# Kernel tuning notes

Measured on AMD Instinct MI355X. Metric: run time of the kernel, lower is better.

The kernel has to match this reference:

```python
import jax, jax.numpy as jnp
import numpy as np

B, C, Ci, V = 1024, 256, 128, 90
EPS = 1e-5


def setup_inputs() -> dict:
    key = jax.random.key(0)
    ks = iter(jax.random.split(key, 40))
    def nrm(shape, s=1.0):
        return jax.random.normal(next(ks), shape, jnp.float32) * s
    def uni(shape):
        return jax.random.uniform(next(ks), shape, jnp.float32, 0.5, 1.5)
    inp = {"x1": nrm((B, C, V)), "x2": nrm((B, C, V))}
    for p in ["g", "th", "ph"]:
        inp[p + "_bn_gamma"] = uni((C,))
        inp[p + "_bn_beta"] = nrm((C,), 0.1)
        inp[p + "_bn_mean"] = nrm((C,), 0.1)
        inp[p + "_bn_var"] = uni((C,))
        inp[p + "_w"] = nrm((Ci, C), 0.05)
        inp[p + "_b"] = nrm((Ci,), 0.05)
    inp["W_w"] = nrm((C, Ci), 0.05)
    inp["W_b"] = nrm((C,), 0.05)
    inp["W_bn_gamma"] = uni((C,))
    inp["W_bn_beta"] = nrm((C,), 0.1)
    inp["W_bn_mean"] = nrm((C,), 0.1)
    inp["W_bn_var"] = uni((C,))
    inp["qt_w"] = nrm((Ci, C), 0.05); inp["qt_b"] = nrm((Ci,), 0.05)
    inp["ks_w"] = nrm((Ci, V), 0.05); inp["ks_b"] = nrm((Ci,), 0.05)
    inp["qs_w"] = nrm((Ci, V), 0.05); inp["qs_b"] = nrm((Ci,), 0.05)
    inp["kt_w"] = nrm((Ci, C), 0.05); inp["kt_b"] = nrm((Ci,), 0.05)
    return inp


def _bn(x, g, b, m, v):
    # eval-mode BatchNorm1d over channel dim of (B, C, V)
    return (x - m[:, None]) * jax.lax.rsqrt(v[:, None] + EPS) * g[:, None] + b[:, None]


def _conv1(x, w, b):
    # 1x1 Conv1d: (B, Cin, V) x (Cout, Cin) -> (B, Cout, V)
    return jnp.einsum('bcv,oc->bov', x, w) + b[:, None]


def reference(x1, x2,
              g_bn_gamma, g_bn_beta, g_bn_mean, g_bn_var, g_w, g_b,
              th_bn_gamma, th_bn_beta, th_bn_mean, th_bn_var, th_w, th_b,
              ph_bn_gamma, ph_bn_beta, ph_bn_mean, ph_bn_var, ph_w, ph_b,
              W_w, W_b, W_bn_gamma, W_bn_beta, W_bn_mean, W_bn_var,
              qt_w, qt_b, ks_w, ks_b, qs_w, qs_b, kt_w, kt_b):
    g_x1 = _conv1(_bn(x1, g_bn_gamma, g_bn_beta, g_bn_mean, g_bn_var), g_w, g_b)
    g_x2 = _conv1(_bn(x2, g_bn_gamma, g_bn_beta, g_bn_mean, g_bn_var), g_w, g_b)
    theta = _conv1(_bn(x1, th_bn_gamma, th_bn_beta, th_bn_mean, th_bn_var), th_w, th_b)  # theta(x1)
    phi = _conv1(_bn(x2, ph_bn_gamma, ph_bn_beta, ph_bn_mean, ph_bn_var), ph_w, ph_b)    # phi(x2)

    e_time = jnp.einsum('biv,bjv->bij', theta, phi)   # (B, Ci, Ci) = theta_x1 @ phi_x2
    e_space = jnp.einsum('bci,bcj->bij', theta, phi)  # (B, V, V)  = theta_x2 @ phi_x1

    attn_time_1 = jax.nn.softmax(e_time, axis=-1)
    attn_time_2 = jax.nn.softmax(jnp.swapaxes(e_time, 1, 2), axis=-1)
    attn_space_2 = jax.nn.softmax(e_space, axis=-1)
    attn_space_1 = jax.nn.softmax(jnp.swapaxes(e_space, 1, 2), axis=-1)

    z1 = jnp.einsum('bij,bjv,bvw->biw', attn_time_2, g_x1, attn_space_2)  # (B, Ci, V)
    z2 = jnp.einsum('bij,bjv,bvw->biw', attn_time_1, g_x2, attn_space_1)

    m1t = x1.mean(axis=2)                      # (B, C)
    q_time = m1t @ qt_w.T + qt_b               # (B, Ci)
    k_space = x2.mean(axis=1) @ ks_w.T + ks_b  # (B, Ci)
    # bmm of (B,1,Ci) x (B,Ci,1) -> (B,1,1); softmax over singleton dim == 1 (kept for faithfulness)
    attn_t2s = jax.nn.softmax(jnp.sum(q_time * k_space, axis=-1, keepdims=True)[:, :, None], axis=-1)
    x2n = x2 + attn_t2s * m1t[:, :, None]      # broadcast (B,1,1)*(B,C,1) over V

    q_space = x1.mean(axis=1) @ qs_w.T + qs_b  # (B, Ci)
    k_time = x2n.mean(axis=2) @ kt_w.T + kt_b  # (B, Ci)
    attn_s2t = jax.nn.softmax(jnp.sum(q_space * k_time, axis=-1, keepdims=True)[:, :, None], axis=-1)
    x1n = x1 + attn_s2t * x2n.mean(axis=1)[:, None, :]

    def Wop(z):
        return _bn(_conv1(z, W_w, W_b), W_bn_gamma, W_bn_beta, W_bn_mean, W_bn_var)

    return (x1n + Wop(z1), x2n + Wop(z2))
```

## Files before the change

kernel.cpp:

```cpp
#include <hip/hip_runtime.h>

namespace {

constexpr int B = 1024;

using u16 = unsigned short;
using u32 = unsigned int;

typedef __attribute__((ext_vector_type(8))) short bf16x8;
typedef __attribute__((ext_vector_type(4))) float f32x4;

#define MFMA16(a, b, c) __builtin_amdgcn_mfma_f32_16x16x32_bf16(a, b, c, 0, 0, 0)

__device__ __forceinline__ u16 f2bf(float f) {
  u32 u = __builtin_bit_cast(u32, f);
  u += 0x7FFFu + ((u >> 16) & 1u);
  return (u16)(u >> 16);
}
__device__ __forceinline__ float bf2f(u16 s) {
  u32 u = ((u32)s) << 16;
  return __builtin_bit_cast(float, u);
}
__device__ __forceinline__ u32 packbf2(float a, float b) {
  return (u32)f2bf(a) | ((u32)f2bf(b) << 16);
}

__global__ __launch_bounds__(256) void k0_fold(
    const float* __restrict__ gg, const float* __restrict__ gbe, const float* __restrict__ gme, const float* __restrict__ gva,
    const float* __restrict__ gw, const float* __restrict__ gbi,
    const float* __restrict__ tg, const float* __restrict__ tbe, const float* __restrict__ tme, const float* __restrict__ tva,
    const float* __restrict__ tw, const float* __restrict__ tbi,
    const float* __restrict__ pg, const float* __restrict__ pbe, const float* __restrict__ pme, const float* __restrict__ pva,
    const float* __restrict__ pw, const float* __restrict__ pbi,
    const float* __restrict__ Ww, const float* __restrict__ Wb,
    const float* __restrict__ Wg2, const float* __restrict__ Wbe, const float* __restrict__ Wme, const float* __restrict__ Wva,
    u16* __restrict__ wgo, float* __restrict__ bgo,
    u16* __restrict__ wthi, u16* __restrict__ wtlo, float* __restrict__ bto,
    u16* __restrict__ wphi, u16* __restrict__ wplo, float* __restrict__ bpo,
    u16* __restrict__ wWo, float* __restrict__ bWo)
{
  __shared__ float red[4];
  const int blk = blockIdx.x, tid = threadIdx.x;
  if (blk < 384) {
    const int p = blk >> 7, o = blk & 127;
    const float *ga, *be, *me, *va, *wm, *bi;
    if (p == 0)      { ga = gg; be = gbe; me = gme; va = gva; wm = gw; bi = gbi; }
    else if (p == 1) { ga = tg; be = tbe; me = tme; va = tva; wm = tw; bi = tbi; }
    else             { ga = pg; be = pbe; me = pme; va = pva; wm = pw; bi = pbi; }
    float s = ga[tid] * rsqrtf(va[tid] + 1e-5f);
    float t = be[tid] - me[tid] * s;
    float wv = wm[o * 256 + tid];
    float val = wv * s;
    if (p == 0) {
      wgo[o * 256 + tid] = f2bf(val);
    } else {
      u16 hi = f2bf(val);
      u16 lo = f2bf(val - bf2f(hi));
      if (p == 1) { wthi[o * 256 + tid] = hi; wtlo[o * 256 + tid] = lo; }
      else        { wphi[o * 256 + tid] = hi; wplo[o * 256 + tid] = lo; }
    }
    float part = t * wv;
#pragma unroll
    for (int off = 32; off; off >>= 1) part += __shfl_down(part, off);
    if ((tid & 63) == 0) red[tid >> 6] = part;
    __syncthreads();
    if (tid == 0) {
      float bsum = bi[o] + red[0] + red[1] + red[2] + red[3];
      if (p == 0) bgo[o] = bsum; else if (p == 1) bto[o] = bsum; else bpo[o] = bsum;
    }
  } else {
    const int c = blk - 384;
    float sW = Wg2[c] * rsqrtf(Wva[c] + 1e-5f);
    if (tid < 128) wWo[c * 128 + tid] = f2bf(Ww[c * 128 + tid] * sW);
    if (tid == 0) bWo[c] = Wb[c] * sW + Wbe[c] - Wme[c] * sW;
  }
}

__global__ __launch_bounds__(512) void k1_conv(
    const float* __restrict__ x1, const float* __restrict__ x2,
    const u16* __restrict__ wG, const float* __restrict__ bG,
    const u16* __restrict__ wTh, const u16* __restrict__ wTl, const float* __restrict__ bT,
    const u16* __restrict__ wPh, const u16* __restrict__ wPl, const float* __restrict__ bP,
    float* __restrict__ thT, float* __restrict__ phT,
    u16* __restrict__ gout,
    float* __restrict__ m1t, float* __restrict__ x2cm, float* __restrict__ x1am)
{
  __shared__ u16 xhi[96 * 264];
  __shared__ u16 xlo[96 * 264];
  __shared__ float red[8];
  const int b = blockIdx.x, tid = threadIdx.x;
  const int l = tid & 63, wv = tid >> 6;
  const int lr = l & 15, lq = l >> 4;
  const int c = tid >> 1, h = tid & 1;

  const float* xb1 = x1 + (size_t)b * 23040;
  const float* xb2 = x2 + (size_t)b * 23040;
  u16* g1d = gout + (size_t)b * 46080;
  u16* g2d = gout + (size_t)(1024 + b) * 46080;
  float* thTb = thT + (size_t)b * 11520;
  float* phTb = phT + (size_t)b * 11520;

  const f32x4 zero = {0.f, 0.f, 0.f, 0.f};

  auto stage = [&](const float* __restrict__ xb) -> float {
    float s = 0.f;
    const int v2lo = h ? 23 : 0, v2hi = h ? 45 : 23;
    for (int v2 = v2lo; v2 < v2hi; ++v2) {
      float2 f = *(const float2*)(xb + c * 90 + 2 * v2);
      s += f.x + f.y;
      u16 h0 = f2bf(f.x);
      xhi[(2 * v2) * 264 + c] = h0;
      xlo[(2 * v2) * 264 + c] = f2bf(f.x - bf2f(h0));
      u16 h1 = f2bf(f.y);
      xhi[(2 * v2 + 1) * 264 + c] = h1;
      xlo[(2 * v2 + 1) * 264 + c] = f2bf(f.y - bf2f(h1));
    }
    for (int i = tid; i < 1536; i += 512) {
      int v = 90 + (i >> 8), cc = i & 255;
      xhi[v * 264 + cc] = 0; xlo[v * 264 + cc] = 0;
    }
    return s;
  };

  auto convSplit = [&](const u16* __restrict__ Wh, const u16* __restrict__ Wl,
                       const float* __restrict__ bias, float* __restrict__ dstF) {
    const int mt = wv;
    f32x4 acc[6];
#pragma unroll
    for (int i = 0; i < 6; ++i) acc[i] = zero;
#pragma unroll
    for (int kk = 0; kk < 8; ++kk) {
      bf16x8 ah = *(const bf16x8*)(Wh + (16 * mt + lr) * 256 + kk * 32 + 8 * lq);
      bf16x8 al = *(const bf16x8*)(Wl + (16 * mt + lr) * 256 + kk * 32 + 8 * lq);
#pragma unroll
      for (int nt = 0; nt < 6; ++nt) {
        bf16x8 bh = *(const bf16x8*)&xhi[(16 * nt + lr) * 264 + kk * 32 + 8 * lq];
        bf16x8 bl = *(const bf16x8*)&xlo[(16 * nt + lr) * 264 + kk * 32 + 8 * lq];
        acc[nt] = MFMA16(ah, bh, acc[nt]);
        acc[nt] = MFMA16(ah, bl, acc[nt]);
        acc[nt] = MFMA16(al, bh, acc[nt]);
      }
    }
    const int c0 = 16 * mt + 4 * lq;
    const float4 b4 = *(const float4*)(bias + c0);
#pragma unroll
    for (int nt = 0; nt < 6; ++nt) {
      const int v = 16 * nt + lr;
      if (v < 90) {
        float4 o;
        o.x = acc[nt][0] + b4.x; o.y = acc[nt][1] + b4.y;
        o.z = acc[nt][2] + b4.z; o.w = acc[nt][3] + b4.w;
        *(float4*)(dstF + v * 128 + c0) = o;
      }
    }
  };

  auto convG = [&](const u16* __restrict__ Wm, const float* __restrict__ bias, u16* __restrict__ dst) {
    const int mt = wv;
    f32x4 acc[6];
#pragma unroll
    for (int i = 0; i < 6; ++i) acc[i] = zero;
#pragma unroll
    for (int kk = 0; kk < 8; ++kk) {
      bf16x8 a = *(const bf16x8*)(Wm + (16 * mt + lr) * 256 + kk * 32 + 8 * lq);
#pragma unroll
      for (int nt = 0; nt < 6; ++nt) {
        bf16x8 bb = *(const bf16x8*)&xhi[(16 * nt + lr) * 264 + kk * 32 + 8 * lq];
        acc[nt] = MFMA16(a, bb, acc[nt]);
      }
    }
    const int c0 = 16 * mt + 4 * lq;
    const float4 b4 = *(const float4*)(bias + c0);
#pragma unroll
    for (int nt = 0; nt < 6; ++nt) {
      const int v = 16 * nt + lr;
      uint2 pk;
      if (v < 90) {
        pk.x = packbf2(acc[nt][0] + b4.x, acc[nt][1] + b4.y);
        pk.y = packbf2(acc[nt][2] + b4.z, acc[nt][3] + b4.w);
      } else { pk.x = 0u; pk.y = 0u; }
      *(uint2*)(dst + v * 128 + c0) = pk;
    }
  };

  {
    float s = stage(xb1);
    float s2 = s + __shfl_down(s, 1);
    if (h == 0) m1t[b * 256 + c] = s2 * (1.f / 90.f);
    float t = s;
#pragma unroll
    for (int o = 32; o; o >>= 1) t += __shfl_down(t, o);
    if (l == 0) red[wv] = t;
  }
  __syncthreads();
  if (tid == 0) {
    float a = 0.f;
#pragma unroll
    for (int i = 0; i < 8; ++i) a += red[i];
    x1am[b] = a * (1.f / 23040.f);
  }
  convSplit(wTh, wTl, bT, thTb);
  convG(wG, bG, g1d);
  __syncthreads();
  stage(xb2);
  __syncthreads();
  if (tid < 96) {
    float s = 0.f;
    for (int cc = 0; cc < 256; ++cc)
      s += bf2f(xhi[tid * 264 + cc]) + bf2f(xlo[tid * 264 + cc]);
    x2cm[b * 96 + tid] = s * (1.f / 256.f);
  }
  convSplit(wPh, wPl, bP, phTb);
  convG(wG, bG, g2d);
}

__global__ __launch_bounds__(256) void k2_attn(
    const float* __restrict__ thTg_, const float* __restrict__ phTg_,
    u16* __restrict__ At1g, u16* __restrict__ At2g,
    u16* __restrict__ As1g, u16* __restrict__ As2g)
{
  __shared__ __align__(16) char smem[108544];
  u16* s0 = (u16*)smem;
  float* st = (float*)(smem + 106496);
  float* eL = (float*)smem;

  const int b = blockIdx.x, tid = threadIdx.x;
  const int l = tid & 63, wv = tid >> 6, lr = l & 15, lq = l >> 4;
  const float* thg = thTg_ + (size_t)b * 11520;
  const float* phg = phTg_ + (size_t)b * 11520;
  const f32x4 zero = {0.f, 0.f, 0.f, 0.f};

  u16* th_hi = s0;
  u16* th_lo = s0 + 13312;
  u16* ph_hi = s0 + 26624;
  u16* ph_lo = s0 + 39936;
  for (int d = tid; d < 2880; d += 256) {
    int v = d >> 5, cq = d & 31;
    float4 t4 = *(const float4*)(thg + v * 128 + 4 * cq);
    float4 p4 = *(const float4*)(phg + v * 128 + 4 * cq);
    float ta[4] = {t4.x, t4.y, t4.z, t4.w};
    float pa[4] = {p4.x, p4.y, p4.z, p4.w};
#pragma unroll
    for (int k = 0; k < 4; ++k) {
      int ci = 4 * cq + k;
      u16 thh = f2bf(ta[k]);
      th_hi[ci * 104 + v] = thh;
      th_lo[ci * 104 + v] = f2bf(ta[k] - bf2f(thh));
      u16 phh = f2bf(pa[k]);
      ph_hi[ci * 104 + v] = phh;
      ph_lo[ci * 104 + v] = f2bf(pa[k] - bf2f(phh));
    }
  }
  for (int d = tid; d < 768; d += 256) {
    int ci = d / 6, v = 90 + d % 6;
    th_hi[ci * 104 + v] = 0; th_lo[ci * 104 + v] = 0;
    ph_hi[ci * 104 + v] = 0; ph_lo[ci * 104 + v] = 0;
  }
  __syncthreads();
  f32x4 accT[2][8];
#pragma unroll
  for (int mi = 0; mi < 2; ++mi)
#pragma unroll
    for (int nt = 0; nt < 8; ++nt) accT[mi][nt] = zero;
#pragma unroll
  for (int mi = 0; mi < 2; ++mi) {
    const int mt = 2 * wv + mi;
#pragma unroll
    for (int kk = 0; kk < 3; ++kk) {
      bf16x8 ah = *(const bf16x8*)&th_hi[(16 * mt + lr) * 104 + kk * 32 + 8 * lq];
      bf16x8 al = *(const bf16x8*)&th_lo[(16 * mt + lr) * 104 + kk * 32 + 8 * lq];
#pragma unroll
      for (int nt = 0; nt < 8; ++nt) {
        bf16x8 bh = *(const bf16x8*)&ph_hi[(16 * nt + lr) * 104 + kk * 32 + 8 * lq];
        bf16x8 bl = *(const bf16x8*)&ph_lo[(16 * nt + lr) * 104 + kk * 32 + 8 * lq];
        accT[mi][nt] = MFMA16(ah, bh, accT[mi][nt]);
        accT[mi][nt] = MFMA16(ah, bl, accT[mi][nt]);
        accT[mi][nt] = MFMA16(al, bh, accT[mi][nt]);
      }
    }
  }
  __syncthreads();
#pragma unroll
  for (int mi = 0; mi < 2; ++mi) {
    const int mt = 2 * wv + mi;
#pragma unroll
    for (int nt = 0; nt < 8; ++nt)
#pragma unroll
      for (int r = 0; r < 4; ++r)
        eL[(16 * nt + lr) * 133 + 16 * mt + 4 * lq + r] = accT[mi][nt][r];
  }
  __syncthreads();
  if (tid < 128) {
    int j = tid; float m = -1e30f;
    for (int i = 0; i < 128; ++i) m = fmaxf(m, eL[j * 133 + i]);
    float s = 0.f;
    for (int i = 0; i < 128; ++i) s += __expf(eL[j * 133 + i] - m);
    st[j] = m; st[128 + j] = 1.f / s;
  } else {
    int i = tid - 128; float m = -1e30f;
    for (int j = 0; j < 128; ++j) m = fmaxf(m, eL[j * 133 + i]);
    float s = 0.f;
    for (int j = 0; j < 128; ++j) s += __expf(eL[j * 133 + i] - m);
    st[256 + i] = m; st[384 + i] = 1.f / s;
  }
  __syncthreads();
  {
    u32* A1 = (u32*)(At1g + (size_t)b * 16384);
    u32* A2 = (u32*)(At2g + (size_t)b * 16384);
    for (int d = tid; d < 8192; d += 256) {
      int i = d >> 6, jp = d & 63;
      float m1 = st[256 + i], s1 = st[384 + i];
      float a0 = __expf(eL[(2 * jp) * 133 + i] - m1) * s1;
      float a1 = __expf(eL[(2 * jp + 1) * 133 + i] - m1) * s1;
      A1[d] = packbf2(a0, a1);
      float m2 = st[i], s2 = st[128 + i];
      float b0 = __expf(eL[i * 133 + 2 * jp] - m2) * s2;
      float b1 = __expf(eL[i * 133 + 2 * jp + 1] - m2) * s2;
      A2[d] = packbf2(b0, b1);
    }
  }
  __syncthreads();

  u16* tTh = s0;
  u16* tTl = s0 + 13056;
  u16* pTh = s0 + 26112;
  u16* pTl = s0 + 39168;
  for (int d = tid; d < 2880; d += 256) {
    int v = d >> 5, cq = d & 31;
    float4 t4 = *(const float4*)(thg + v * 128 + 4 * cq);
    float4 p4 = *(const float4*)(phg + v * 128 + 4 * cq);
    float ta[4] = {t4.x, t4.y, t4.z, t4.w};
    float pa[4] = {p4.x, p4.y, p4.z, p4.w};
    u16 th_h[4], th_l[4], ph_h[4], ph_l[4];
#pragma unroll
    for (int k = 0; k < 4; ++k) {
      th_h[k] = f2bf(ta[k]); th_l[k] = f2bf(ta[k] - bf2f(th_h[k]));
      ph_h[k] = f2bf(pa[k]); ph_l[k] = f2bf(pa[k] - bf2f(ph_h[k]));
    }
    uint2 w0, w1;
    w0.x = (u32)th_h[0] | ((u32)th_h[1] << 16); w0.y = (u32)th_h[2] | ((u32)th_h[3] << 16);
    *(uint2*)&tTh[v * 136 + 4 * cq] = w0;
    w1.x = (u32)th_l[0] | ((u32)th_l[1] << 16); w1.y = (u32)th_l[2] | ((u32)th_l[3] << 16);
    *(uint2*)&tTl[v * 136 + 4 * cq] = w1;
    w0.x = (u32)ph_h[0] | ((u32)ph_h[1] << 16); w0.y = (u32)ph_h[2] | ((u32)ph_h[3] << 16);
    *(uint2*)&pTh[v * 136 + 4 * cq] = w0;
    w1.x = (u32)ph_l[0] | ((u32)ph_l[1] << 16); w1.y = (u32)ph_l[2] | ((u32)ph_l[3] << 16);
    *(uint2*)&pTl[v * 136 + 4 * cq] = w1;
  }
  for (int d = tid; d < 192; d += 256) {
    int v = 90 + (d >> 5), cq = d & 31;
    uint2 z; z.x = 0u; z.y = 0u;
    *(uint2*)&tTh[v * 136 + 4 * cq] = z;
    *(uint2*)&tTl[v * 136 + 4 * cq] = z;
    *(uint2*)&pTh[v * 136 + 4 * cq] = z;
    *(uint2*)&pTl[v * 136 + 4 * cq] = z;
  }
  __syncthreads();
  f32x4 accS[9];
#pragma unroll
  for (int it = 0; it < 9; ++it) accS[it] = zero;
#pragma unroll
  for (int it = 0; it < 9; ++it) {
    const int t5 = wv + 4 * it;
    const int mt = t5 / 6, nt = t5 - 6 * (t5 / 6);
#pragma unroll
    for (int kk = 0; kk < 4; ++kk) {
      bf16x8 ah = *(const bf16x8*)&tTh[(16 * mt + lr) * 136 + kk * 32 + 8 * lq];
      bf16x8 al = *(const bf16x8*)&tTl[(16 * mt + lr) * 136 + kk * 32 + 8 * lq];
      bf16x8 bh = *(const bf16x8*)&pTh[(16 * nt + lr) * 136 + kk * 32 + 8 * lq];
      bf16x8 bl = *(const bf16x8*)&pTl[(16 * nt + lr) * 136 + kk * 32 + 8 * lq];
      accS[it] = MFMA16(ah, bh, accS[it]);
      accS[it] = MFMA16(ah, bl, accS[it]);
      accS[it] = MFMA16(al, bh, accS[it]);
    }
  }
  __syncthreads();
  {
    float* esL = (float*)smem;
#pragma unroll
    for (int it = 0; it < 9; ++it) {
      const int t5 = wv + 4 * it;
      const int mt = t5 / 6, nt = t5 - 6 * (t5 / 6);
#pragma unroll
      for (int r = 0; r < 4; ++r)
        esL[(16 * nt + lr) * 101 + 16 * mt + 4 * lq + r] = accS[it][r];
    }
  }
  __syncthreads();
  {
    float* esL = (float*)smem;
    if (tid < 96) {
      int v = tid; float m = -1e30f;
      for (int w2 = 0; w2 < 90; ++w2) m = fmaxf(m, esL[v * 101 + w2]);
      float s = 0.f;
      for (int w2 = 0; w2 < 90; ++w2) s += __expf(esL[v * 101 + w2] - m);
      st[v] = m; st[128 + v] = 1.f / s;
    } else if (tid >= 128 && tid < 224) {
      int v = tid - 128; float m = -1e30f;
      for (int w2 = 0; w2 < 90; ++w2) m = fmaxf(m, esL[w2 * 101 + v]);
      float s = 0.f;
      for (int w2 = 0; w2 < 90; ++w2) s += __expf(esL[w2 * 101 + v] - m);
      st[256 + v] = m; st[384 + v] = 1.f / s;
    }
  }
  __syncthreads();
  {
    float* esL = (float*)smem;
    u32* S1 = (u32*)(As1g + (size_t)b * 9216);
    u32* S2 = (u32*)(As2g + (size_t)b * 9216);
    for (int d = tid; d < 4608; d += 256) {
      int w2 = d / 48, vp = d - (d / 48) * 48;
      int v0 = 2 * vp, v1 = 2 * vp + 1;
      float a0 = __expf(esL[v0 * 101 + w2] - st[v0]) * st[128 + v0];
      float a1 = __expf(esL[v1 * 101 + w2] - st[v1]) * st[128 + v1];
      S1[d] = packbf2(a0, a1);
      float b0 = __expf(esL[w2 * 101 + v0] - st[256 + v0]) * st[384 + v0];
      float b1 = __expf(esL[w2 * 101 + v1] - st[256 + v1]) * st[384 + v1];
      S2[d] = packbf2(b0, b1);
    }
  }
}

__global__ __launch_bounds__(256) void k3_out(
    const float* __restrict__ x1, const float* __restrict__ x2,
    const u16* __restrict__ At1g, const u16* __restrict__ At2g,
    const u16* __restrict__ As1g, const u16* __restrict__ As2g,
    const u16* __restrict__ wW, const float* __restrict__ bW,
    const float* __restrict__ m1t, const float* __restrict__ x2cm, const float* __restrict__ x1am,
    float* __restrict__ out)
{
  __shared__ u16 gT[96 * 136];
  __shared__ u16 Tb[128 * 104];
  __shared__ u16 ZT[96 * 136];
  const int b = blockIdx.x, tid = threadIdx.x;
  const int l = tid & 63, wv = tid >> 6, lr = l & 15, lq = l >> 4;
  const f32x4 zero = {0.f, 0.f, 0.f, 0.f};

  float* out1 = out + (size_t)b * 23040;
  float* out2 = out + (size_t)23040 * 1024 + (size_t)b * 23040;
  const u16* g1s = (const u16*)out1;
  const u16* g2s = (const u16*)out2;

  auto phase = [&](const u16* __restrict__ gsrc, const u16* __restrict__ At,
                   const u16* __restrict__ AsT, const float* __restrict__ xres,
                   float* __restrict__ dst, bool modeA) {
    for (int i = tid; i < 1536; i += 256) {
      int v = i >> 4, hh = i & 15;
      *(uint4*)&gT[v * 136 + 8 * hh] = ((const uint4*)gsrc)[i];
    }
    __syncthreads();
#pragma unroll
    for (int ni = 0; ni < 2; ++ni) {
      const int nt = 2 * wv + ni;
      f32x4 acc[6];
#pragma unroll
      for (int i = 0; i < 6; ++i) acc[i] = zero;
#pragma unroll
      for (int kk = 0; kk < 4; ++kk) {
        bf16x8 bb = *(const bf16x8*)(At + (16 * nt + lr) * 128 + kk * 32 + 8 * lq);
#pragma unroll
        for (int mt = 0; mt < 6; ++mt) {
          bf16x8 a = *(const bf16x8*)&gT[(16 * mt + lr) * 136 + kk * 32 + 8 * lq];
          acc[mt] = MFMA16(a, bb, acc[mt]);
        }
      }
#pragma unroll
      for (int mt = 0; mt < 6; ++mt) {
        uint2 pk;
        pk.x = packbf2(acc[mt][0], acc[mt][1]);
        pk.y = packbf2(acc[mt][2], acc[mt][3]);
        *(uint2*)&Tb[(16 * nt + lr) * 104 + 16 * mt + 4 * lq] = pk;
      }
    }
    __syncthreads();
    {
      f32x4 acc[2][6];
#pragma unroll
      for (int i = 0; i < 2; ++i)
#pragma unroll
        for (int j = 0; j < 6; ++j) acc[i][j] = zero;
#pragma unroll
      for (int kk = 0; kk < 3; ++kk) {
        bf16x8 a0 = *(const bf16x8*)&Tb[(16 * (2 * wv) + lr) * 104 + kk * 32 + 8 * lq];
        bf16x8 a1 = *(const bf16x8*)&Tb[(16 * (2 * wv + 1) + lr) * 104 + kk * 32 + 8 * lq];
#pragma unroll
        for (int nt = 0; nt < 6; ++nt) {
          bf16x8 bb = *(const bf16x8*)(AsT + (16 * nt + lr) * 96 + kk * 32 + 8 * lq);
          acc[0][nt] = MFMA16(a0, bb, acc[0][nt]);
          acc[1][nt] = MFMA16(a1, bb, acc[1][nt]);
        }
      }
#pragma unroll
      for (int mi = 0; mi < 2; ++mi) {
        const int mt = 2 * wv + mi;
#pragma unroll
        for (int nt = 0; nt < 6; ++nt) {
          uint2 pk;
          pk.x = packbf2(acc[mi][nt][0], acc[mi][nt][1]);
          pk.y = packbf2(acc[mi][nt][2], acc[mi][nt][3]);
          *(uint2*)&ZT[(16 * nt + lr) * 136 + 16 * mt + 4 * lq] = pk;
        }
      }
    }
    __syncthreads();
    const float am = modeA ? 0.f : x1am[b];
#pragma unroll
    for (int mi = 0; mi < 4; ++mi) {
      const int mt = 4 * wv + mi;
      f32x4 acc[6];
#pragma unroll
      for (int i = 0; i < 6; ++i) acc[i] = zero;
#pragma unroll
      for (int kk = 0; kk < 4; ++kk) {
        bf16x8 a = *(const bf16x8*)(wW + (16 * mt + lr) * 128 + kk * 32 + 8 * lq);
#pragma unroll
        for (int nt = 0; nt < 6; ++nt) {
          bf16x8 bb = *(const bf16x8*)&ZT[(16 * nt + lr) * 136 + kk * 32 + 8 * lq];
          acc[nt] = MFMA16(a, bb, acc[nt]);
        }
      }
      const int c0 = 16 * mt + 4 * lq;
      const float4 bw4 = *(const float4*)(bW + c0);
      float bwA[4] = {bw4.x, bw4.y, bw4.z, bw4.w};
      float mA[4] = {0.f, 0.f, 0.f, 0.f};
      if (modeA) {
        const float4 m4 = *(const float4*)(m1t + b * 256 + c0);
        mA[0] = m4.x; mA[1] = m4.y; mA[2] = m4.z; mA[3] = m4.w;
      }
#pragma unroll
      for (int nt = 0; nt < 6; ++nt) {
        const int v = 16 * nt + lr;
        if (v < 90) {
          const float addv = modeA ? 0.f : (am + x2cm[b * 96 + v]);
#pragma unroll
          for (int r = 0; r < 4; ++r) {
            const int c = c0 + r;
            const float extra = modeA ? mA[r] : addv;
            dst[c * 90 + v] = xres[c * 90 + v] + acc[nt][r] + bwA[r] + extra;
          }
        }
      }
    }
    __syncthreads();
  };

  phase(g2s, At1g + (size_t)b * 16384, As1g + (size_t)b * 9216,
        x2 + (size_t)b * 23040, out2, true);
  phase(g1s, At2g + (size_t)b * 16384, As2g + (size_t)b * 9216,
        x1 + (size_t)b * 23040, out1, false);
}

}

extern "C" void kernel_launch(void* const* d_in, const int* in_sizes, int n_in,
                              void* d_out, int out_size, void* d_ws, size_t ws_size,
                              hipStream_t stream)
{
  (void)in_sizes; (void)n_in; (void)out_size; (void)ws_size;
  const float* x1  = (const float*)d_in[0];
  const float* x2  = (const float*)d_in[1];
  const float* gg  = (const float*)d_in[2];
  const float* gbe = (const float*)d_in[3];
  const float* gme = (const float*)d_in[4];
  const float* gva = (const float*)d_in[5];
  const float* gw  = (const float*)d_in[6];
  const float* gbi = (const float*)d_in[7];
  const float* tg  = (const float*)d_in[8];
  const float* tbe = (const float*)d_in[9];
  const float* tme = (const float*)d_in[10];
  const float* tva = (const float*)d_in[11];
  const float* tw  = (const float*)d_in[12];
  const float* tbi = (const float*)d_in[13];
  const float* pg  = (const float*)d_in[14];
  const float* pbe = (const float*)d_in[15];
  const float* pme = (const float*)d_in[16];
  const float* pva = (const float*)d_in[17];
  const float* pw  = (const float*)d_in[18];
  const float* pbi = (const float*)d_in[19];
  const float* Ww  = (const float*)d_in[20];
  const float* Wb  = (const float*)d_in[21];
  const float* Wg  = (const float*)d_in[22];
  const float* Wbe = (const float*)d_in[23];
  const float* Wme = (const float*)d_in[24];
  const float* Wva = (const float*)d_in[25];

  float* out = (float*)d_out;
  unsigned char* W8 = (unsigned char*)d_ws;

  size_t off = 0;
  auto al = [&](size_t n) { size_t r = off; off += (n + 255) & ~(size_t)255; return r; };
  const size_t oWG  = al(65536);
  const size_t oWTh = al(65536), oWTl = al(65536);
  const size_t oWPh = al(65536), oWPl = al(65536);
  const size_t oWW  = al(65536);
  const size_t oBG = al(512), oBT = al(512), oBP = al(512), oBW = al(1024);
  const size_t oTH = al((size_t)B * 46080), oPH = al((size_t)B * 46080);
  const size_t oA1 = al((size_t)B * 32768), oA2 = al((size_t)B * 32768);
  const size_t oS1 = al((size_t)B * 18432), oS2 = al((size_t)B * 18432);
  const size_t oM1 = al((size_t)B * 1024), oXC = al((size_t)B * 384), oXA = al((size_t)B * 4);

  k0_fold<<<dim3(640), dim3(256), 0, stream>>>(
      gg, gbe, gme, gva, gw, gbi,
      tg, tbe, tme, tva, tw, tbi,
      pg, pbe, pme, pva, pw, pbi,
      Ww, Wb, Wg, Wbe, Wme, Wva,
      (u16*)(W8 + oWG), (float*)(W8 + oBG),
      (u16*)(W8 + oWTh), (u16*)(W8 + oWTl), (float*)(W8 + oBT),
      (u16*)(W8 + oWPh), (u16*)(W8 + oWPl), (float*)(W8 + oBP),
      (u16*)(W8 + oWW), (float*)(W8 + oBW));

  k1_conv<<<dim3(B), dim3(512), 0, stream>>>(
      x1, x2,
      (const u16*)(W8 + oWG), (const float*)(W8 + oBG),
      (const u16*)(W8 + oWTh), (const u16*)(W8 + oWTl), (const float*)(W8 + oBT),
      (const u16*)(W8 + oWPh), (const u16*)(W8 + oWPl), (const float*)(W8 + oBP),
      (float*)(W8 + oTH), (float*)(W8 + oPH),
      (u16*)out,
      (float*)(W8 + oM1), (float*)(W8 + oXC), (float*)(W8 + oXA));

  k2_attn<<<dim3(B), dim3(256), 0, stream>>>(
      (const float*)(W8 + oTH), (const float*)(W8 + oPH),
      (u16*)(W8 + oA1), (u16*)(W8 + oA2),
      (u16*)(W8 + oS1), (u16*)(W8 + oS2));

  k3_out<<<dim3(B), dim3(256), 0, stream>>>(
      x1, x2,
      (const u16*)(W8 + oA1), (const u16*)(W8 + oA2),
      (const u16*)(W8 + oS1), (const u16*)(W8 + oS2),
      (const u16*)(W8 + oWW), (const float*)(W8 + oBW),
      (const float*)(W8 + oM1), (const float*)(W8 + oXC), (const float*)(W8 + oXA),
      out);
}
```

Measured before the change: 463.9 us.

## Restage conv in channel halves, emit pre-split bf16 theta/phi, widen attention kernel

k1_conv now stages x in two 128-channel halves through a smaller shared buffer, allowing more blocks per CU, and fuses the theta/phi and g convolutions into one MFMA loop. It writes theta/phi already split into packed bf16 hi/lo words in two layouts: channel-major in workspace and v-major in spare space of the output buffer. This removes the fp32 reload and resplitting in k2_attn. k2_attn moves to 512 threads, and the spatial attention maps are stored inside the output buffer instead of separate workspace, relying on k3 reading them before it overwrites that region.

```diff
diff --git a/kernel.cpp b/kernel.cpp
--- a/kernel.cpp
+++ b/kernel.cpp
@@ -76,148 +76,144 @@
   }
 }
 
-__global__ __launch_bounds__(512) void k1_conv(
+__global__ __launch_bounds__(512, 4) void k1_conv(
     const float* __restrict__ x1, const float* __restrict__ x2,
     const u16* __restrict__ wG, const float* __restrict__ bG,
     const u16* __restrict__ wTh, const u16* __restrict__ wTl, const float* __restrict__ bT,
     const u16* __restrict__ wPh, const u16* __restrict__ wPl, const float* __restrict__ bP,
-    float* __restrict__ thT, float* __restrict__ phT,
-    u16* __restrict__ gout,
+    u32* __restrict__ thRm, u32* __restrict__ phRm,
+    u16* __restrict__ outU,
     float* __restrict__ m1t, float* __restrict__ x2cm, float* __restrict__ x1am)
 {
-  __shared__ u16 xhi[96 * 264];
-  __shared__ u16 xlo[96 * 264];
-  __shared__ float red[8];
+  __shared__ u32 qb[64 * 92];
+  __shared__ u16 xh[96 * 136];
+  __shared__ u16 xl[96 * 136];
+  __shared__ float red[4];
   const int b = blockIdx.x, tid = threadIdx.x;
-  const int l = tid & 63, wv = tid >> 6;
-  const int lr = l & 15, lq = l >> 4;
-  const int c = tid >> 1, h = tid & 1;
-
-  const float* xb1 = x1 + (size_t)b * 23040;
-  const float* xb2 = x2 + (size_t)b * 23040;
-  u16* g1d = gout + (size_t)b * 46080;
-  u16* g2d = gout + (size_t)(1024 + b) * 46080;
-  float* thTb = thT + (size_t)b * 11520;
-  float* phTb = phT + (size_t)b * 11520;
-
+  const int l = tid & 63, wv = tid >> 6, lr = l & 15, lq = l >> 4;
   const f32x4 zero = {0.f, 0.f, 0.f, 0.f};
 
-  auto stage = [&](const float* __restrict__ xb) -> float {
-    float s = 0.f;
-    const int v2lo = h ? 23 : 0, v2hi = h ? 45 : 23;
-    for (int v2 = v2lo; v2 < v2hi; ++v2) {
-      float2 f = *(const float2*)(xb + c * 90 + 2 * v2);
-      s += f.x + f.y;
-      u16 h0 = f2bf(f.x);
-      xhi[(2 * v2) * 264 + c] = h0;
-      xlo[(2 * v2) * 264 + c] = f2bf(f.x - bf2f(h0));
-      u16 h1 = f2bf(f.y);
-      xhi[(2 * v2 + 1) * 264 + c] = h1;
-      xlo[(2 * v2 + 1) * 264 + c] = f2bf(f.y - bf2f(h1));
-    }
-    for (int i = tid; i < 1536; i += 512) {
-      int v = 90 + (i >> 8), cc = i & 255;
-      xhi[v * 264 + cc] = 0; xlo[v * 264 + cc] = 0;
-    }
-    return s;
-  };
-
-  auto convSplit = [&](const u16* __restrict__ Wh, const u16* __restrict__ Wl,
-                       const float* __restrict__ bias, float* __restrict__ dstF) {
-    const int mt = wv;
-    f32x4 acc[6];
-#pragma unroll
-    for (int i = 0; i < 6; ++i) acc[i] = zero;
-#pragma unroll
-    for (int kk = 0; kk < 8; ++kk) {
-      bf16x8 ah = *(const bf16x8*)(Wh + (16 * mt + lr) * 256 + kk * 32 + 8 * lq);
-      bf16x8 al = *(const bf16x8*)(Wl + (16 * mt + lr) * 256 + kk * 32 + 8 * lq);
-#pragma unroll
-      for (int nt = 0; nt < 6; ++nt) {
-        bf16x8 bh = *(const bf16x8*)&xhi[(16 * nt + lr) * 264 + kk * 32 + 8 * lq];
-        bf16x8 bl = *(const bf16x8*)&xlo[(16 * nt + lr) * 264 + kk * 32 + 8 * lq];
-        acc[nt] = MFMA16(ah, bh, acc[nt]);
-        acc[nt] = MFMA16(ah, bl, acc[nt]);
-        acc[nt] = MFMA16(al, bh, acc[nt]);
-      }
-    }
-    const int c0 = 16 * mt + 4 * lq;
-    const float4 b4 = *(const float4*)(bias + c0);
+  auto doPhase = [&](const float* __restrict__ xb,
+                     const u16* __restrict__ Wh, const u16* __restrict__ Wl, const float* __restrict__ biasT,
+                     u32* __restrict__ rmDst, u32* __restrict__ pkDst, u16* __restrict__ gDst, bool isX1) {
+    f32x4 aT[6], aG[6];
+#pragma unroll
+    for (int i = 0; i < 6; ++i) { aT[i] = zero; aG[i] = zero; }
+    float cs = 0.f;
+    for (int h = 0; h < 2; ++h) {
+      for (int q = 0; q < 2; ++q) {
+        __syncthreads();
+        const float* src = xb + (2 * h + q) * 5760;
+        for (int t = tid; t < 2880; t += 512) {
+          float2 f = *(const float2*)(src + 2 * t);
+          int cl = (2 * t) / 90, v = 2 * t - 90 * cl;
+          u16 h0 = f2bf(f.x); u16 l0 = f2bf(f.x - bf2f(h0));
+          u16 h1 = f2bf(f.y); u16 l1 = f2bf(f.y - bf2f(h1));
+          uint2 w; w.x = (u32)h0 | ((u32)l0 << 16); w.y = (u32)h1 | ((u32)l1 << 16);
+          *(uint2*)&qb[cl * 92 + v] = w;
+        }
+        __syncthreads();
+        for (int t = tid; t < 1440; t += 512) {
+          int v = t % 90, c4 = t / 90;
+          u32 p0 = qb[(4 * c4 + 0) * 92 + v], p1 = qb[(4 * c4 + 1) * 92 + v];
+          u32 p2 = qb[(4 * c4 + 2) * 92 + v], p3 = qb[(4 * c4 + 3) * 92 + v];
+          uint2 hi, lo;
+          hi.x = (p0 & 0xFFFFu) | (p1 << 16);
+          hi.y = (p2 & 0xFFFFu) | (p3 << 16);
+          lo.x = (p0 >> 16) | (p1 & 0xFFFF0000u);
+          lo.y = (p2 >> 16) | (p3 & 0xFFFF0000u);
+          int base = v * 136 + 64 * q + 4 * c4;
+          *(uint2*)&xh[base] = hi;
+          *(uint2*)&xl[base] = lo;
+        }
+        if (q == 1) {
+          for (int t = tid; t < 384; t += 512) {
+            int v = 90 + (t >> 6), c2 = (t & 63) * 2;
+            *(u32*)&xh[v * 136 + c2] = 0u;
+            *(u32*)&xl[v * 136 + c2] = 0u;
+          }
+        }
+      }
+      __syncthreads();
+      if (isX1) {
+        if (tid < 128) {
+          float s = 0.f;
+          for (int v = 0; v < 90; ++v) s += bf2f(xh[v * 136 + tid]) + bf2f(xl[v * 136 + tid]);
+          m1t[b * 256 + 128 * h + tid] = s * (1.f / 90.f);
+#pragma unroll
+          for (int o = 32; o; o >>= 1) s += __shfl_down(s, o);
+          if ((tid & 63) == 0) red[(tid >> 6) + 2 * h] = s;
+        }
+      } else {
+        if (tid < 90) {
+          float s = 0.f;
+          for (int cl = 0; cl < 128; ++cl) s += bf2f(xh[tid * 136 + cl]) + bf2f(xl[tid * 136 + cl]);
+          cs += s;
+        }
+      }
+      for (int kk = 0; kk < 4; ++kk) {
+        const int wo = (16 * wv + lr) * 256 + 128 * h + kk * 32 + 8 * lq;
+        bf16x8 ah = *(const bf16x8*)(Wh + wo);
+        bf16x8 al = *(const bf16x8*)(Wl + wo);
+        bf16x8 ag = *(const bf16x8*)(wG + wo);
+#pragma unroll
+        for (int nt = 0; nt < 6; ++nt) {
+          const int bo = (16 * nt + lr) * 136 + kk * 32 + 8 * lq;
+          bf16x8 bh = *(const bf16x8*)&xh[bo];
+          bf16x8 bl = *(const bf16x8*)&xl[bo];
+          aT[nt] = MFMA16(ah, bh, aT[nt]);
+          aT[nt] = MFMA16(ah, bl, aT[nt]);
+          aT[nt] = MFMA16(al, bh, aT[nt]);
+          aG[nt] = MFMA16(ag, bh, aG[nt]);
+        }
+      }
+    }
+    __syncthreads();
+    const int c0 = 16 * wv + 4 * lq;
+    const float4 bt4 = *(const float4*)(biasT + c0);
+    const float4 bg4 = *(const float4*)(bG + c0);
 #pragma unroll
     for (int nt = 0; nt < 6; ++nt) {
       const int v = 16 * nt + lr;
+      u32 pk0, pk1, pk2, pk3; uint2 gpk;
       if (v < 90) {
-        float4 o;
-        o.x = acc[nt][0] + b4.x; o.y = acc[nt][1] + b4.y;
-        o.z = acc[nt][2] + b4.z; o.w = acc[nt][3] + b4.w;
-        *(float4*)(dstF + v * 128 + c0) = o;
-      }
+        float t0 = aT[nt][0] + bt4.x, t1 = aT[nt][1] + bt4.y;
+        float t2 = aT[nt][2] + bt4.z, t3 = aT[nt][3] + bt4.w;
+        u16 h0 = f2bf(t0), h1 = f2bf(t1), h2 = f2bf(t2), h3 = f2bf(t3);
+        pk0 = (u32)h0 | ((u32)f2bf(t0 - bf2f(h0)) << 16);
+        pk1 = (u32)h1 | ((u32)f2bf(t1 - bf2f(h1)) << 16);
+        pk2 = (u32)h2 | ((u32)f2bf(t2 - bf2f(h2)) << 16);
+        pk3 = (u32)h3 | ((u32)f2bf(t3 - bf2f(h3)) << 16);
+        gpk.x = packbf2(aG[nt][0] + bg4.x, aG[nt][1] + bg4.y);
+        gpk.y = packbf2(aG[nt][2] + bg4.z, aG[nt][3] + bg4.w);
+      } else { pk0 = pk1 = pk2 = pk3 = 0u; gpk.x = 0u; gpk.y = 0u; }
+      uint4 q4; q4.x = pk0; q4.y = pk1; q4.z = pk2; q4.w = pk3;
+      *(uint4*)(pkDst + v * 128 + c0) = q4;
+      rmDst[(c0 + 0) * 96 + v] = pk0;
+      rmDst[(c0 + 1) * 96 + v] = pk1;
+      rmDst[(c0 + 2) * 96 + v] = pk2;
+      rmDst[(c0 + 3) * 96 + v] = pk3;
+      *(uint2*)(gDst + v * 128 + c0) = gpk;
+    }
+    if (isX1) {
+      if (tid == 0) x1am[b] = (red[0] + red[1] + red[2] + red[3]) * (1.f / 23040.f);
+    } else {
+      if (tid < 90) x2cm[b * 96 + tid] = cs * (1.f / 256.f);
     }
   };
 
-  auto convG = [&](const u16* __restrict__ Wm, const float* __restrict__ bias, u16* __restrict__ dst) {
-    const int mt = wv;
-    f32x4 acc[6];
-#pragma unroll
-    for (int i = 0; i < 6; ++i) acc[i] = zero;
-#pragma unroll
-    for (int kk = 0; kk < 8; ++kk) {
-      bf16x8 a = *(const bf16x8*)(Wm + (16 * mt + lr) * 256 + kk * 32 + 8 * lq);
-#pragma unroll
-      for (int nt = 0; nt < 6; ++nt) {
-        bf16x8 bb = *(const bf16x8*)&xhi[(16 * nt + lr) * 264 + kk * 32 + 8 * lq];
-        acc[nt] = MFMA16(a, bb, acc[nt]);
-      }
-    }
-    const int c0 = 16 * mt + 4 * lq;
-    const float4 b4 = *(const float4*)(bias + c0);
-#pragma unroll
-    for (int nt = 0; nt < 6; ++nt) {
-      const int v = 16 * nt + lr;
-      uint2 pk;
-      if (v < 90) {
-        pk.x = packbf2(acc[nt][0] + b4.x, acc[nt][1] + b4.y);
-        pk.y = packbf2(acc[nt][2] + b4.z, acc[nt][3] + b4.w);
-      } else { pk.x = 0u; pk.y = 0u; }
-      *(uint2*)(dst + v * 128 + c0) = pk;
-    }
-  };
-
-  {
-    float s = stage(xb1);
-    float s2 = s + __shfl_down(s, 1);
-    if (h == 0) m1t[b * 256 + c] = s2 * (1.f / 90.f);
-    float t = s;
-#pragma unroll
-    for (int o = 32; o; o >>= 1) t += __shfl_down(t, o);
-    if (l == 0) red[wv] = t;
-  }
-  __syncthreads();
-  if (tid == 0) {
-    float a = 0.f;
-#pragma unroll
-    for (int i = 0; i < 8; ++i) a += red[i];
-    x1am[b] = a * (1.f / 23040.f);
-  }
-  convSplit(wTh, wTl, bT, thTb);
-  convG(wG, bG, g1d);
-  __syncthreads();
-  stage(xb2);
-  __syncthreads();
-  if (tid < 96) {
-    float s = 0.f;
-    for (int cc = 0; cc < 256; ++cc)
-      s += bf2f(xhi[tid * 264 + cc]) + bf2f(xlo[tid * 264 + cc]);
-    x2cm[b * 96 + tid] = s * (1.f / 256.f);
-  }
-  convSplit(wPh, wPl, bP, phTb);
-  convG(wG, bG, g2d);
-}
-
-__global__ __launch_bounds__(256) void k2_attn(
-    const float* __restrict__ thTg_, const float* __restrict__ phTg_,
-    u16* __restrict__ At1g, u16* __restrict__ At2g,
-    u16* __restrict__ As1g, u16* __restrict__ As2g)
+  u16* o1 = outU + (size_t)b * 46080;
+  u16* o2 = outU + (size_t)(1024 + b) * 46080;
+  doPhase(x1 + (size_t)b * 23040, wTh, wTl, bT,
+          thRm + (size_t)b * 12288, (u32*)(o1 + 12288), o1, true);
+  doPhase(x2 + (size_t)b * 23040, wPh, wPl, bP,
+          phRm + (size_t)b * 12288, (u32*)(o2 + 12288), o2, false);
+}
+
+__global__ __launch_bounds__(512) void k2_attn(
+    const u32* __restrict__ thRm, const u32* __restrict__ phRm,
+    u16* __restrict__ outU,
+    u16* __restrict__ At1g, u16* __restrict__ At2g)
 {
   __shared__ __align__(16) char smem[108544];
   u16* s0 = (u16*)smem;
@@ -226,69 +222,57 @@
 
   const int b = blockIdx.x, tid = threadIdx.x;
   const int l = tid & 63, wv = tid >> 6, lr = l & 15, lq = l >> 4;
-  const float* thg = thTg_ + (size_t)b * 11520;
-  const float* phg = phTg_ + (size_t)b * 11520;
   const f32x4 zero = {0.f, 0.f, 0.f, 0.f};
+
+  const u32* thRmB = thRm + (size_t)b * 12288;
+  const u32* phRmB = phRm + (size_t)b * 12288;
+  const u32* thPk = (const u32*)(outU + (size_t)b * 46080 + 12288);
+  const u32* phPk = (const u32*)(outU + (size_t)(1024 + b) * 46080 + 12288);
+  u32* S1 = (u32*)(outU + (size_t)(1024 + b) * 46080 + 36864);
+  u32* S2 = (u32*)(outU + (size_t)b * 46080 + 36864);
 
   u16* th_hi = s0;
   u16* th_lo = s0 + 13312;
   u16* ph_hi = s0 + 26624;
   u16* ph_lo = s0 + 39936;
-  for (int d = tid; d < 2880; d += 256) {
-    int v = d >> 5, cq = d & 31;
-    float4 t4 = *(const float4*)(thg + v * 128 + 4 * cq);
-    float4 p4 = *(const float4*)(phg + v * 128 + 4 * cq);
-    float ta[4] = {t4.x, t4.y, t4.z, t4.w};
-    float pa[4] = {p4.x, p4.y, p4.z, p4.w};
-#pragma unroll
-    for (int k = 0; k < 4; ++k) {
-      int ci = 4 * cq + k;
-      u16 thh = f2bf(ta[k]);
-      th_hi[ci * 104 + v] = thh;
-      th_lo[ci * 104 + v] = f2bf(ta[k] - bf2f(thh));
-      u16 phh = f2bf(pa[k]);
-      ph_hi[ci * 104 + v] = phh;
-      ph_lo[ci * 104 + v] = f2bf(pa[k] - bf2f(phh));
-    }
-  }
-  for (int d = tid; d < 768; d += 256) {
-    int ci = d / 6, v = 90 + d % 6;
-    th_hi[ci * 104 + v] = 0; th_lo[ci * 104 + v] = 0;
-    ph_hi[ci * 104 + v] = 0; ph_lo[ci * 104 + v] = 0;
-  }
-  __syncthreads();
-  f32x4 accT[2][8];
-#pragma unroll
-  for (int mi = 0; mi < 2; ++mi)
-#pragma unroll
-    for (int nt = 0; nt < 8; ++nt) accT[mi][nt] = zero;
-#pragma unroll
-  for (int mi = 0; mi < 2; ++mi) {
-    const int mt = 2 * wv + mi;
-#pragma unroll
-    for (int kk = 0; kk < 3; ++kk) {
-      bf16x8 ah = *(const bf16x8*)&th_hi[(16 * mt + lr) * 104 + kk * 32 + 8 * lq];
-      bf16x8 al = *(const bf16x8*)&th_lo[(16 * mt + lr) * 104 + kk * 32 + 8 * lq];
-#pragma unroll
-      for (int nt = 0; nt < 8; ++nt) {
-        bf16x8 bh = *(const bf16x8*)&ph_hi[(16 * nt + lr) * 104 + kk * 32 + 8 * lq];
-        bf16x8 bl = *(const bf16x8*)&ph_lo[(16 * nt + lr) * 104 + kk * 32 + 8 * lq];
-        accT[mi][nt] = MFMA16(ah, bh, accT[mi][nt]);
-        accT[mi][nt] = MFMA16(ah, bl, accT[mi][nt]);
-        accT[mi][nt] = MFMA16(al, bh, accT[mi][nt]);
-      }
-    }
-  }
-  __syncthreads();
-#pragma unroll
-  for (int mi = 0; mi < 2; ++mi) {
-    const int mt = 2 * wv + mi;
-#pragma unroll
-    for (int nt = 0; nt < 8; ++nt)
-#pragma unroll
-      for (int r = 0; r < 4; ++r)
-        eL[(16 * nt + lr) * 133 + 16 * mt + 4 * lq + r] = accT[mi][nt][r];
-  }
+  for (int d = tid; d < 6144; d += 512) {
+    int ten = (d >= 3072);
+    int i = d - 3072 * ten;
+    int ci = i / 24, q4 = i - 24 * ci;
+    uint4 P = *(const uint4*)((ten ? phRmB : thRmB) + ci * 96 + 4 * q4);
+    uint2 hi, lo;
+    hi.x = (P.x & 0xFFFFu) | (P.y << 16);
+    hi.y = (P.z & 0xFFFFu) | (P.w << 16);
+    lo.x = (P.x >> 16) | (P.y & 0xFFFF0000u);
+    lo.y = (P.z >> 16) | (P.w & 0xFFFF0000u);
+    *(uint2*)((ten ? ph_hi : th_hi) + ci * 104 + 4 * q4) = hi;
+    *(uint2*)((ten ? ph_lo : th_lo) + ci * 104 + 4 * q4) = lo;
+  }
+  __syncthreads();
+  f32x4 acc[8];
+#pragma unroll
+  for (int nt = 0; nt < 8; ++nt) acc[nt] = zero;
+#pragma unroll
+  for (int kk = 0; kk < 3; ++kk) {
+    const int ao = (16 * wv + lr) * 104 + kk * 32 + 8 * lq;
+    bf16x8 ah = *(const bf16x8*)&th_hi[ao];
+    bf16x8 al = *(const bf16x8*)&th_lo[ao];
+#pragma unroll
+    for (int nt = 0; nt < 8; ++nt) {
+      const int bo = (16 * nt + lr) * 104 + kk * 32 + 8 * lq;
+      bf16x8 bh = *(const bf16x8*)&ph_hi[bo];
+      bf16x8 bl = *(const bf16x8*)&ph_lo[bo];
+      acc[nt] = MFMA16(ah, bh, acc[nt]);
+      acc[nt] = MFMA16(ah, bl, acc[nt]);
+      acc[nt] = MFMA16(al, bh, acc[nt]);
+    }
+  }
+  __syncthreads();
+#pragma unroll
+  for (int nt = 0; nt < 8; ++nt)
+#pragma unroll
+    for (int r = 0; r < 4; ++r)
+      eL[(16 * nt + lr) * 133 + 16 * wv + 4 * lq + r] = acc[nt][r];
   __syncthreads();
   if (tid < 128) {
     int j = tid; float m = -1e30f;
@@ -296,7 +280,7 @@
     float s = 0.f;
     for (int i = 0; i < 128; ++i) s += __expf(eL[j * 133 + i] - m);
     st[j] = m; st[128 + j] = 1.f / s;
-  } else {
+  } else if (tid < 256) {
     int i = tid - 128; float m = -1e30f;
     for (int j = 0; j < 128; ++j) m = fmaxf(m, eL[j * 133 + i]);
     float s = 0.f;
@@ -307,15 +291,15 @@
   {
     u32* A1 = (u32*)(At1g + (size_t)b * 16384);
     u32* A2 = (u32*)(At2g + (size_t)b * 16384);
-    for (int d = tid; d < 8192; d += 256) {
+    for (int d = tid; d < 8192; d += 512) {
       int i = d >> 6, jp = d & 63;
-      float m1 = st[256 + i], s1 = st[384 + i];
-      float a0 = __expf(eL[(2 * jp) * 133 + i] - m1) * s1;
-      float a1 = __expf(eL[(2 * jp + 1) * 133 + i] - m1) * s1;
+      float m1 = st[256 + i], s1v = st[384 + i];
+      float a0 = __expf(eL[(2 * jp) * 133 + i] - m1) * s1v;
+      float a1 = __expf(eL[(2 * jp + 1) * 133 + i] - m1) * s1v;
       A1[d] = packbf2(a0, a1);
-      float m2 = st[i], s2 = st[128 + i];
-      float b0 = __expf(eL[i * 133 + 2 * jp] - m2) * s2;
-      float b1 = __expf(eL[i * 133 + 2 * jp + 1] - m2) * s2;
+      float m2 = st[i], s2v = st[128 + i];
+      float b0 = __expf(eL[i * 133 + 2 * jp] - m2) * s2v;
+      float b1 = __expf(eL[i * 133 + 2 * jp + 1] - m2) * s2v;
       A2[d] = packbf2(b0, b1);
     }
   }
@@ -325,65 +309,54 @@
   u16* tTl = s0 + 13056;
   u16* pTh = s0 + 26112;
   u16* pTl = s0 + 39168;
-  for (int d = tid; d < 2880; d += 256) {
-    int v = d >> 5, cq = d & 31;
-    float4 t4 = *(const float4*)(thg + v * 128 + 4 * cq);
-    float4 p4 = *(const float4*)(phg + v * 128 + 4 * cq);
-    float ta[4] = {t4.x, t4.y, t4.z, t4.w};
-    float pa[4] = {p4.x, p4.y, p4.z, p4.w};
-    u16 th_h[4], th_l[4], ph_h[4], ph_l[4];
-#pragma unroll
-    for (int k = 0; k < 4; ++k) {
-      th_h[k] = f2bf(ta[k]); th_l[k] = f2bf(ta[k] - bf2f(th_h[k]));
-      ph_h[k] = f2bf(pa[k]); ph_l[k] = f2bf(pa[k] - bf2f(ph_h[k]));
-    }
-    uint2 w0, w1;
-    w0.x = (u32)th_h[0] | ((u32)th_h[1] << 16); w0.y = (u32)th_h[2] | ((u32)th_h[3] << 16);
-    *(uint2*)&tTh[v * 136 + 4 * cq] = w0;
-    w1.x = (u32)th_l[0] | ((u32)th_l[1] << 16); w1.y = (u32)th_l[2] | ((u32)th_l[3] << 16);
-    *(uint2*)&tTl[v * 136 + 4 * cq] = w1;
-    w0.x = (u32)ph_h[0] | ((u32)ph_h[1] << 16); w0.y = (u32)ph_h[2] | ((u32)ph_h[3] << 16);
-    *(uint2*)&pTh[v * 136 + 4 * cq] = w0;
-    w1.x = (u32)ph_l[0] | ((u32)ph_l[1] << 16); w1.y = (u32)ph_l[2] | ((u32)ph_l[3] << 16);
-    *(uint2*)&pTl[v * 136 + 4 * cq] = w1;
-  }
-  for (int d = tid; d < 192; d += 256) {
-    int v = 90 + (d >> 5), cq = d & 31;
-    uint2 z; z.x = 0u; z.y = 0u;
-    *(uint2*)&tTh[v * 136 + 4 * cq] = z;
-    *(uint2*)&tTl[v * 136 + 4 * cq] = z;
-    *(uint2*)&pTh[v * 136 + 4 * cq] = z;
-    *(uint2*)&pTl[v * 136 + 4 * cq] = z;
-  }
-  __syncthreads();
-  f32x4 accS[9];
-#pragma unroll
-  for (int it = 0; it < 9; ++it) accS[it] = zero;
-#pragma unroll
-  for (int it = 0; it < 9; ++it) {
-    const int t5 = wv + 4 * it;
-    const int mt = t5 / 6, nt = t5 - 6 * (t5 / 6);
-#pragma unroll
-    for (int kk = 0; kk < 4; ++kk) {
-      bf16x8 ah = *(const bf16x8*)&tTh[(16 * mt + lr) * 136 + kk * 32 + 8 * lq];
-      bf16x8 al = *(const bf16x8*)&tTl[(16 * mt + lr) * 136 + kk * 32 + 8 * lq];
-      bf16x8 bh = *(const bf16x8*)&pTh[(16 * nt + lr) * 136 + kk * 32 + 8 * lq];
-      bf16x8 bl = *(const bf16x8*)&pTl[(16 * nt + lr) * 136 + kk * 32 + 8 * lq];
-      accS[it] = MFMA16(ah, bh, accS[it]);
-      accS[it] = MFMA16(ah, bl, accS[it]);
-      accS[it] = MFMA16(al, bh, accS[it]);
+  for (int d = tid; d < 6144; d += 512) {
+    int ten = (d >= 3072);
+    int i = d - 3072 * ten;
+    int v = i >> 5, q4 = i & 31;
+    uint4 P = *(const uint4*)((ten ? phPk : thPk) + v * 128 + 4 * q4);
+    uint2 hi, lo;
+    hi.x = (P.x & 0xFFFFu) | (P.y << 16);
+    hi.y = (P.z & 0xFFFFu) | (P.w << 16);
+    lo.x = (P.x >> 16) | (P.y & 0xFFFF0000u);
+    lo.y = (P.z >> 16) | (P.w & 0xFFFF0000u);
+    *(uint2*)((ten ? pTh : tTh) + v * 136 + 4 * q4) = hi;
+    *(uint2*)((ten ? pTl : tTl) + v * 136 + 4 * q4) = lo;
+  }
+  __syncthreads();
+  f32x4 accS[5];
+#pragma unroll
+  for (int it = 0; it < 5; ++it) accS[it] = zero;
+#pragma unroll
+  for (int it = 0; it < 5; ++it) {
+    const int t5 = wv + 8 * it;
+    if (t5 < 36) {
+      const int mt = t5 / 6, nt = t5 - 6 * (t5 / 6);
+#pragma unroll
+      for (int kk = 0; kk < 4; ++kk) {
+        const int ao = (16 * mt + lr) * 136 + kk * 32 + 8 * lq;
+        const int bo = (16 * nt + lr) * 136 + kk * 32 + 8 * lq;
+        bf16x8 ah = *(const bf16x8*)&tTh[ao];
+        bf16x8 al = *(const bf16x8*)&tTl[ao];
+        bf16x8 bh = *(const bf16x8*)&pTh[bo];
+        bf16x8 bl = *(const bf16x8*)&pTl[bo];
+        accS[it] = MFMA16(ah, bh, accS[it]);
+        accS[it] = MFMA16(ah, bl, accS[it]);
+        accS[it] = MFMA16(al, bh, accS[it]);
+      }
     }
   }
   __syncthreads();
   {
     float* esL = (float*)smem;
 #pragma unroll
-    for (int it = 0; it < 9; ++it) {
-      const int t5 = wv + 4 * it;
-      const int mt = t5 / 6, nt = t5 - 6 * (t5 / 6);
-#pragma unroll
-      for (int r = 0; r < 4; ++r)
-        esL[(16 * nt + lr) * 101 + 16 * mt + 4 * lq + r] = accS[it][r];
+    for (int it = 0; it < 5; ++it) {
+      const int t5 = wv + 8 * it;
+      if (t5 < 36) {
+        const int mt = t5 / 6, nt = t5 - 6 * (t5 / 6);
+#pragma unroll
+        for (int r = 0; r < 4; ++r)
+          esL[(16 * nt + lr) * 101 + 16 * mt + 4 * lq + r] = accS[it][r];
+      }
     }
   }
   __syncthreads();
@@ -406,11 +379,9 @@
   __syncthreads();
   {
     float* esL = (float*)smem;
-    u32* S1 = (u32*)(As1g + (size_t)b * 9216);
-    u32* S2 = (u32*)(As2g + (size_t)b * 9216);
-    for (int d = tid; d < 4608; d += 256) {
-      int w2 = d / 48, vp = d - (d / 48) * 48;
-      int v0 = 2 * vp, v1 = 2 * vp + 1;
+    for (int d = tid; d < 4608; d += 512) {
+      int w2 = d / 48, vp = d - 48 * (d / 48);
+      int v0 = 2 * vp, v1 = v0 + 1;
       float a0 = __expf(esL[v0 * 101 + w2] - st[v0]) * st[128 + v0];
       float a1 = __expf(esL[v1 * 101 + w2] - st[v1]) * st[128 + v1];
       S1[d] = packbf2(a0, a1);
@@ -424,7 +395,6 @@
 __global__ __launch_bounds__(256) void k3_out(
     const float* __restrict__ x1, const float* __restrict__ x2,
     const u16* __restrict__ At1g, const u16* __restrict__ At2g,
-    const u16* __restrict__ As1g, const u16* __restrict__ As2g,
     const u16* __restrict__ wW, const float* __restrict__ bW,
     const float* __restrict__ m1t, const float* __restrict__ x2cm, const float* __restrict__ x1am,
     float* __restrict__ out)
@@ -440,6 +410,8 @@
   float* out2 = out + (size_t)23040 * 1024 + (size_t)b * 23040;
   const u16* g1s = (const u16*)out1;
   const u16* g2s = (const u16*)out2;
+  const u16* As1 = (const u16*)out2 + 36864;
+  const u16* As2 = (const u16*)out1 + 36864;
 
   auto phase = [&](const u16* __restrict__ gsrc, const u16* __restrict__ At,
                    const u16* __restrict__ AsT, const float* __restrict__ xres,
@@ -544,10 +516,8 @@
     __syncthreads();
   };
 
-  phase(g2s, At1g + (size_t)b * 16384, As1g + (size_t)b * 9216,
-        x2 + (size_t)b * 23040, out2, true);
-  phase(g1s, At2g + (size_t)b * 16384, As2g + (size_t)b * 9216,
-        x1 + (size_t)b * 23040, out1, false);
+  phase(g2s, At1g + (size_t)b * 16384, As1, x2 + (size_t)b * 23040, out2, true);
+  phase(g1s, At2g + (size_t)b * 16384, As2, x1 + (size_t)b * 23040, out1, false);
 }
 
 }
@@ -594,9 +564,8 @@
   const size_t oWPh = al(65536), oWPl = al(65536);
   const size_t oWW  = al(65536);
   const size_t oBG = al(512), oBT = al(512), oBP = al(512), oBW = al(1024);
-  const size_t oTH = al((size_t)B * 46080), oPH = al((size_t)B * 46080);
+  const size_t oRM1 = al((size_t)B * 49152), oRM2 = al((size_t)B * 49152);
   const size_t oA1 = al((size_t)B * 32768), oA2 = al((size_t)B * 32768);
-  const size_t oS1 = al((size_t)B * 18432), oS2 = al((size_t)B * 18432);
   const size_t oM1 = al((size_t)B * 1024), oXC = al((size_t)B * 384), oXA = al((size_t)B * 4);
 
   k0_fold<<<dim3(640), dim3(256), 0, stream>>>(
@@ -614,19 +583,18 @@
       (const u16*)(W8 + oWG), (const float*)(W8 + oBG),
       (const u16*)(W8 + oWTh), (const u16*)(W8 + oWTl), (const float*)(W8 + oBT),
       (const u16*)(W8 + oWPh), (const u16*)(W8 + oWPl), (const float*)(W8 + oBP),
-      (float*)(W8 + oTH), (float*)(W8 + oPH),
+      (u32*)(W8 + oRM1), (u32*)(W8 + oRM2),
       (u16*)out,
       (float*)(W8 + oM1), (float*)(W8 + oXC), (float*)(W8 + oXA));
 
-  k2_attn<<<dim3(B), dim3(256), 0, stream>>>(
-      (const float*)(W8 + oTH), (const float*)(W8 + oPH),
-      (u16*)(W8 + oA1), (u16*)(W8 + oA2),
-      (u16*)(W8 + oS1), (u16*)(W8 + oS2));
+  k2_attn<<<dim3(B), dim3(512), 0, stream>>>(
+      (const u32*)(W8 + oRM1), (const u32*)(W8 + oRM2),
+      (u16*)out,
+      (u16*)(W8 + oA1), (u16*)(W8 + oA2));
 
   k3_out<<<dim3(B), dim3(256), 0, stream>>>(
       x1, x2,
       (const u16*)(W8 + oA1), (const u16*)(W8 + oA2),
-      (const u16*)(W8 + oS1), (const u16*)(W8 + oS2),
       (const u16*)(W8 + oWW), (const float*)(W8 + oBW),
       (const float*)(W8 + oM1), (const float*)(W8 + oXC), (const float*)(W8 + oXA),
       out);
```

New measurement: 450.5 us. 2.9% less time.
